# Optimization experiments

Hardware: AMD Instinct MI355X
Metric: run time of the kernel (lower is better)

The kernel has to match this reference:

```python
import jax, jax.numpy as jnp
import numpy as np

ALPHA = 0.2    # LeakyReLU negative slope (init arg alpha)
HEADS = 8
EPS = 1e-5     # LayerNorm eps


def setup_inputs() -> dict:
    key = jax.random.key(0)
    ks = jax.random.split(key, 16)
    B, S, D = 4, 1024, 256
    dh = D // HEADS  # 32
    x = jax.random.normal(ks[0], (B, S, D), jnp.float32)
    adj = (jax.random.uniform(ks[1], (B, S, S)) < 0.05).astype(jnp.float32)
    adj = jnp.maximum(adj, jnp.eye(S, dtype=jnp.float32)[None])

    def w(k, shape, fan):
        return jax.random.normal(k, shape, jnp.float32) * (fan ** -0.5)

    # GAT layer 0: in->hidden (concat heads)
    W0 = w(ks[2], (D, D), D); a_src0 = w(ks[3], (HEADS, dh), dh); a_dst0 = w(ks[4], (HEADS, dh), dh)
    # GAT layer 1: hidden->hidden (concat heads)
    W1 = w(ks[5], (D, D), D); a_src1 = w(ks[6], (HEADS, dh), dh); a_dst1 = w(ks[7], (HEADS, dh), dh)
    # GAT layer 2: hidden->out (mean over heads, head_dim = out_dim)
    W2 = w(ks[8], (D, HEADS * D), D); a_src2 = w(ks[9], (HEADS, D), D); a_dst2 = w(ks[10], (HEADS, D), D)
    # LayerNorm
    ln_g = jnp.ones((D,), jnp.float32); ln_b = jnp.zeros((D,), jnp.float32)
    # FFN: D -> 2D -> D
    ff_w1 = w(ks[11], (D, 2 * D), D); ff_b1 = jnp.zeros((2 * D,), jnp.float32)
    ff_w2 = w(ks[12], (2 * D, D), 2 * D); ff_b2 = jnp.zeros((D,), jnp.float32)
    return dict(adj=adj, x=x, W0=W0, a_src0=a_src0, a_dst0=a_dst0,
                W1=W1, a_src1=a_src1, a_dst1=a_dst1,
                W2=W2, a_src2=a_src2, a_dst2=a_dst2,
                ln_g=ln_g, ln_b=ln_b,
                ff_w1=ff_w1, ff_b1=ff_b1, ff_w2=ff_w2, ff_b2=ff_b2)


def _gat_layer(h, adj, W, a_src, a_dst, concat):
    B, S, _ = h.shape
    hp = jnp.einsum('bsi,io->bso', h, W).reshape(B, S, HEADS, -1)  # [B,S,H,dh]
    src = jnp.einsum('bshd,hd->bsh', hp, a_src)  # per-node source score
    dst = jnp.einsum('bshd,hd->bsh', hp, a_dst)  # per-node dest score
    # e[b,i,j,h] = LeakyReLU(src_i + dst_j), masked by adjacency
    e = jax.nn.leaky_relu(src[:, :, None, :] + dst[:, None, :, :], ALPHA)
    e = jnp.where(adj[..., None] > 0, e, jnp.float32(-1e9))
    attn = jax.nn.softmax(e, axis=2)  # softmax over neighbors j
    out = jnp.einsum('bijh,bjhd->bihd', attn, hp)
    return out.reshape(B, S, -1) if concat else out.mean(axis=2)


def reference(adj, x, W0, a_src0, a_dst0, W1, a_src1, a_dst1, W2, a_src2, a_dst2,
              ln_g, ln_b, ff_w1, ff_b1, ff_w2, ff_b2):
    # MultiAttentionGAT: 3 layers with residuals, ELU between layers
    h = jax.nn.elu(_gat_layer(x, adj, W0, a_src0, a_dst0, True) + x)
    h = jax.nn.elu(_gat_layer(h, adj, W1, a_src1, a_dst1, True) + h)
    h = _gat_layer(h, adj, W2, a_src2, a_dst2, False) + h
    # LayerNorm
    mu = h.mean(-1, keepdims=True)
    var = h.var(-1, keepdims=True)
    h = (h - mu) * jax.lax.rsqrt(var + EPS) * ln_g + ln_b
    # GELU FFN + residual
    ff = jnp.dot(jax.nn.gelu(jnp.dot(h, ff_w1) + ff_b1), ff_w2) + ff_b2
    return h + ff
```

## Files before the change

### kernel.cpp

```cpp
#include <hip/hip_runtime.h>
#include <hip/hip_bf16.h>

#define B_ 4
#define S_ 1024
#define D_ 256
#define H_ 8
#define LRELU_ALPHA 0.2f
#define MAXDEG 128

typedef __attribute__((ext_vector_type(8))) short short8;
typedef __attribute__((ext_vector_type(4))) float floatx4;

__device__ __forceinline__ float bf2f(unsigned short u) {
    union { unsigned int i; float f; } c; c.i = ((unsigned int)u) << 16; return c.f;
}
__device__ __forceinline__ unsigned short f2bf(float f) {
    union { float f; unsigned int u; } c; c.f = f;
    unsigned int r = (c.u + 0x7FFF + ((c.u >> 16) & 1)) >> 16;
    return (unsigned short)r;
}

__device__ void castT_body(const float* __restrict__ W, unsigned short* __restrict__ out,
                           int K, int N, int k0, int n0, float (*t)[33], int tid) {
    int tx = tid & 31, ty = tid >> 5;
#pragma unroll
    for (int i = 0; i < 4; ++i)
        t[ty + 8 * i][tx] = W[(size_t)(k0 + ty + 8 * i) * N + n0 + tx];
    __syncthreads();
#pragma unroll
    for (int i = 0; i < 4; ++i)
        out[(size_t)(n0 + ty + 8 * i) * K + k0 + tx] = f2bf(t[tx][ty + 8 * i]);
}

__global__ __launch_bounds__(256) void k_prep(
        const float* __restrict__ x, unsigned short* __restrict__ xb,
        const float* __restrict__ W0, unsigned short* __restrict__ W0t,
        const float* __restrict__ W1, unsigned short* __restrict__ W1t,
        const float* __restrict__ W2, unsigned short* __restrict__ W2t,
        const float* __restrict__ F1, unsigned short* __restrict__ F1t,
        const float* __restrict__ F2, unsigned short* __restrict__ F2t,
        const float* __restrict__ as2, const float* __restrict__ ad2,
        float* __restrict__ WS2, float* __restrict__ WD2,
        const float* __restrict__ adj, int* __restrict__ nbr, int* __restrict__ cnt) {
    __shared__ float t[32][33];
    __shared__ int c;
    int b = blockIdx.x, tid = threadIdx.x;
    if (b < 1024) {
        int i = b * 256 + tid;
        float4 v = ((const float4*)x)[i];
        ushort4 u; u.x = f2bf(v.x); u.y = f2bf(v.y); u.z = f2bf(v.z); u.w = f2bf(v.w);
        ((ushort4*)xb)[i] = u;
    } else if (b < 1088) {
        int i = b - 1024; castT_body(W0, W0t, 256, 256, (i & 7) * 32, (i >> 3) * 32, t, tid);
    } else if (b < 1152) {
        int i = b - 1088; castT_body(W1, W1t, 256, 256, (i & 7) * 32, (i >> 3) * 32, t, tid);
    } else if (b < 1664) {
        int i = b - 1152;
        int k0 = (i & 7) * 32, d0 = ((i >> 3) & 7) * 32, h = i >> 6;
        int tx = tid & 31, ty = tid >> 5;
#pragma unroll
        for (int q = 0; q < 4; ++q)
            t[ty + 8 * q][tx] = W2[(size_t)(k0 + ty + 8 * q) * 2048 + h * 256 + d0 + tx];
        __syncthreads();
#pragma unroll
        for (int q = 0; q < 4; ++q)
            W2t[(size_t)(d0 + ty + 8 * q) * 2048 + h * 256 + k0 + tx] = f2bf(t[tx][ty + 8 * q]);
    } else if (b < 1792) {
        int i = b - 1664; castT_body(F1, F1t, 256, 512, (i & 7) * 32, (i >> 3) * 32, t, tid);
    } else if (b < 1920) {
        int i = b - 1792; castT_body(F2, F2t, 512, 256, (i & 15) * 32, (i >> 4) * 32, t, tid);
    } else if (b < 2432) {
        int id = (b - 1920) * 4 + (tid >> 6);
        int h = id >> 8, k = id & 255;
        int lane = tid & 63;
        float4 w4 = *(const float4*)(W2 + (size_t)k * 2048 + h * 256 + lane * 4);
        float4 a4 = *(const float4*)(as2 + h * 256 + lane * 4);
        float4 d4 = *(const float4*)(ad2 + h * 256 + lane * 4);
        float s = w4.x * a4.x + w4.y * a4.y + w4.z * a4.z + w4.w * a4.w;
        float d = w4.x * d4.x + w4.y * d4.y + w4.z * d4.z + w4.w * d4.w;
#pragma unroll
        for (int o = 32; o; o >>= 1) { s += __shfl_xor(s, o); d += __shfl_xor(d, o); }
        if (lane == 0) { WS2[h * 256 + k] = s; WD2[h * 256 + k] = d; }
    } else {
        int row = b - 2432;
        if (tid == 0) c = 0;
        __syncthreads();
        float4 a4 = ((const float4*)(adj + (size_t)row * S_))[tid];
#pragma unroll
        for (int q = 0; q < 4; ++q) {
            float a = q == 0 ? a4.x : q == 1 ? a4.y : q == 2 ? a4.z : a4.w;
            if (a > 0.f) {
                int s = atomicAdd(&c, 1);
                if (s < MAXDEG) nbr[row * MAXDEG + s] = tid * 4 + q;
            }
        }
        __syncthreads();
        if (tid == 0) cnt[row] = c < MAXDEG ? c : MAXDEG;
    }
}

__global__ __launch_bounds__(256) void k_gemm_wide(const unsigned short* __restrict__ A,
        const unsigned short* __restrict__ Bt, float* __restrict__ P,
        int M, int N, int K, int Kc) {
    __shared__ unsigned short As[64][40];
    __shared__ unsigned short Bs[256][40];
    int tid = threadIdx.x;
    int bm = blockIdx.y * 64, bn = blockIdx.x * 256;
    int kbeg = blockIdx.z * Kc, kend = kbeg + Kc;
    int lane = tid & 63, wv = tid >> 6;
    int lrow = lane & 15, lq = lane >> 4;
    floatx4 acc[4][4] = {};
    int sm = tid >> 2, skq = (tid & 3) * 8;
    const unsigned short* Ap = A + (size_t)(bm + sm) * K + skq;
    const unsigned short* Bp0 = Bt + (size_t)(bn + sm) * K + skq;
    const unsigned short* Bp1 = Bp0 + (size_t)64 * K;
    const unsigned short* Bp2 = Bp0 + (size_t)128 * K;
    const unsigned short* Bp3 = Bp0 + (size_t)192 * K;
    short8 av  = *(const short8*)(Ap + kbeg);
    short8 bv0 = *(const short8*)(Bp0 + kbeg);
    short8 bv1 = *(const short8*)(Bp1 + kbeg);
    short8 bv2 = *(const short8*)(Bp2 + kbeg);
    short8 bv3 = *(const short8*)(Bp3 + kbeg);
    for (int k0 = kbeg; k0 < kend; k0 += 32) {
        *(short8*)&As[sm][skq]        = av;
        *(short8*)&Bs[sm][skq]        = bv0;
        *(short8*)&Bs[sm + 64][skq]   = bv1;
        *(short8*)&Bs[sm + 128][skq]  = bv2;
        *(short8*)&Bs[sm + 192][skq]  = bv3;
        __syncthreads();
        if (k0 + 32 < kend) {
            av  = *(const short8*)(Ap + k0 + 32);
            bv0 = *(const short8*)(Bp0 + k0 + 32);
            bv1 = *(const short8*)(Bp1 + k0 + 32);
            bv2 = *(const short8*)(Bp2 + k0 + 32);
            bv3 = *(const short8*)(Bp3 + k0 + 32);
        }
        short8 aF[4], bF[4];
#pragma unroll
        for (int mi = 0; mi < 4; ++mi)
            aF[mi] = *(const short8*)&As[mi * 16 + lrow][lq * 8];
#pragma unroll
        for (int ni = 0; ni < 4; ++ni)
            bF[ni] = *(const short8*)&Bs[wv * 64 + ni * 16 + lrow][lq * 8];
#pragma unroll
        for (int mi = 0; mi < 4; ++mi)
#pragma unroll
            for (int ni = 0; ni < 4; ++ni)
                acc[mi][ni] = __builtin_amdgcn_mfma_f32_16x16x32_bf16(aF[mi], bF[ni], acc[mi][ni], 0, 0, 0);
        __syncthreads();
    }
    float* out = P + (size_t)blockIdx.z * M * N;
#pragma unroll
    for (int mi = 0; mi < 4; ++mi)
#pragma unroll
        for (int ni = 0; ni < 4; ++ni)
#pragma unroll
            for (int r = 0; r < 4; ++r) {
                int grow = bm + mi * 16 + lq * 4 + r;
                int gcol = bn + wv * 64 + ni * 16 + lrow;
                out[(size_t)grow * N + gcol] = acc[mi][ni][r];
            }
}

template<int EPI>
__global__ __launch_bounds__(256) void k_gemm64(
        const unsigned short* __restrict__ A, const unsigned short* __restrict__ Bt,
        int N, int K,
        float* __restrict__ Pout, unsigned short* __restrict__ Ob,
        const float* __restrict__ p1, const float* __restrict__ p2,
        float* __restrict__ SRC, float* __restrict__ DST) {
    __shared__ unsigned short As[2][64][40];
    __shared__ unsigned short Bs[2][64][40];
    int tid = threadIdx.x;
    int bm = blockIdx.y * 64, bn = blockIdx.x * 64;
    int lane = tid & 63, wv = tid >> 6;
    int lrow = lane & 15, lq = lane >> 4;
    floatx4 acc[4] = {};
    int sm = tid >> 2, skq = (tid & 3) * 8;
    const unsigned short* Ap = A + (size_t)(bm + sm) * K + skq;
    const unsigned short* Bp = Bt + (size_t)(bn + sm) * K + skq;
    short8 av = *(const short8*)Ap;
    short8 bv = *(const short8*)Bp;
    *(short8*)&As[0][sm][skq] = av;
    *(short8*)&Bs[0][sm][skq] = bv;
    __syncthreads();
    int cur = 0;
    for (int k0 = 0; k0 < K; k0 += 32) {
        bool more = k0 + 32 < K;
        if (more) {
            av = *(const short8*)(Ap + k0 + 32);
            bv = *(const short8*)(Bp + k0 + 32);
        }
        short8 aF = *(const short8*)&As[cur][wv * 16 + lrow][lq * 8];
        short8 bF[4];
#pragma unroll
        for (int ni = 0; ni < 4; ++ni)
            bF[ni] = *(const short8*)&Bs[cur][ni * 16 + lrow][lq * 8];
#pragma unroll
        for (int ni = 0; ni < 4; ++ni)
            acc[ni] = __builtin_amdgcn_mfma_f32_16x16x32_bf16(aF, bF[ni], acc[ni], 0, 0, 0);
        if (more) {
            *(short8*)&As[cur ^ 1][sm][skq] = av;
            *(short8*)&Bs[cur ^ 1][sm][skq] = bv;
            __syncthreads();
            cur ^= 1;
        }
    }
    int row0 = bm + wv * 16 + lq * 4;
    if (EPI == 0) {
#pragma unroll
        for (int ni = 0; ni < 4; ++ni)
#pragma unroll
            for (int r = 0; r < 4; ++r)
                Ob[(size_t)(row0 + r) * N + bn + ni * 16 + lrow] = f2bf(acc[ni][r]);
        float asv[4], adv[4];
#pragma unroll
        for (int ni = 0; ni < 4; ++ni) {
            asv[ni] = p1[bn + ni * 16 + lrow];
            adv[ni] = p2[bn + ni * 16 + lrow];
        }
#pragma unroll
        for (int r = 0; r < 4; ++r) {
            float sA = acc[0][r] * asv[0] + acc[1][r] * asv[1];
            float sB = acc[2][r] * asv[2] + acc[3][r] * asv[3];
            float dA = acc[0][r] * adv[0] + acc[1][r] * adv[1];
            float dB = acc[2][r] * adv[2] + acc[3][r] * adv[3];
#pragma unroll
            for (int o = 8; o; o >>= 1) {
                sA += __shfl_xor(sA, o); sB += __shfl_xor(sB, o);
                dA += __shfl_xor(dA, o); dB += __shfl_xor(dB, o);
            }
            if (lrow == 0) {
                int h0 = bn >> 5;
                SRC[(row0 + r) * 8 + h0]     = sA;
                SRC[(row0 + r) * 8 + h0 + 1] = sB;
                DST[(row0 + r) * 8 + h0]     = dA;
                DST[(row0 + r) * 8 + h0 + 1] = dB;
            }
        }
    } else if (EPI == 2) {
#pragma unroll
        for (int ni = 0; ni < 4; ++ni) {
            int gcol = bn + ni * 16 + lrow;
            float bb = p1[gcol];
#pragma unroll
            for (int r = 0; r < 4; ++r) {
                float xx = acc[ni][r] + bb;
                float tt = tanhf(0.7978845608028654f * (xx + 0.044715f * xx * xx * xx));
                Ob[(size_t)(row0 + r) * N + gcol] = f2bf(0.5f * xx * (1.f + tt));
            }
        }
    } else if (EPI == 3) {
#pragma unroll
        for (int ni = 0; ni < 4; ++ni) {
            int gcol = bn + ni * 16 + lrow;
            float bb = p1[gcol];
#pragma unroll
            for (int r = 0; r < 4; ++r) {
                float res = p2[(size_t)(row0 + r) * 256 + gcol];
                Pout[(size_t)(row0 + r) * 256 + gcol] = acc[ni][r] + bb + res;
            }
        }
    }
}

__global__ __launch_bounds__(256) void k_attn4(const unsigned short* __restrict__ hp,
        const float* __restrict__ src, const float* __restrict__ dst,
        const int* __restrict__ nbr, const int* __restrict__ cnts,
        const float* __restrict__ X, float* __restrict__ Hout,
        unsigned short* __restrict__ Hb,
        const float* __restrict__ WS2, const float* __restrict__ WD2,
        float* __restrict__ SRC2, float* __restrict__ DST2) {
    int tid = threadIdx.x;
    int rq = tid >> 6;
    int lane = tid & 63;
    int row = blockIdx.x * 4 + rq;
    int rb = row & ~(S_ - 1);
    __shared__ int nb[4][MAXDEG];
    __shared__ float ss[4][8];
    __shared__ float ew[4][MAXDEG * 9];
    int cnt = cnts[row];
    for (int t = lane; t < cnt; t += 64) nb[rq][t] = nbr[row * MAXDEG + t];
    if (lane < 8) ss[rq][lane] = src[row * H_ + lane];
    for (int idx = lane; idx < cnt * 8; idx += 64) {
        int n = idx >> 3, h = idx & 7;
        int j = nb[rq][n];
        float e = ss[rq][h] + dst[(rb + j) * H_ + h];
        ew[rq][n * 9 + h] = e > 0.f ? e : LRELU_ALPHA * e;
    }
    {
        int h = lane >> 3, s8 = lane & 7;
        float m = -1e30f;
        for (int n = s8; n < cnt; n += 8) m = fmaxf(m, ew[rq][n * 9 + h]);
#pragma unroll
        for (int o = 4; o; o >>= 1) m = fmaxf(m, __shfl_xor(m, o));
        float s = 0.f;
        for (int n = s8; n < cnt; n += 8) {
            float v = __expf(ew[rq][n * 9 + h] - m); ew[rq][n * 9 + h] = v; s += v;
        }
#pragma unroll
        for (int o = 4; o; o >>= 1) s += __shfl_xor(s, o);
        float inv = s > 0.f ? 1.f / s : 0.f;
        for (int n = s8; n < cnt; n += 8) ew[rq][n * 9 + h] *= inv;
    }
    int d0 = lane * 4;
    int h = lane >> 3;
    const unsigned short* hpb = hp + (size_t)rb * 256 + d0;
    const float* ewr = ew[rq];
    float A0 = 0.f, A1 = 0.f, A2 = 0.f, A3 = 0.f;
    float B0 = 0.f, B1 = 0.f, B2 = 0.f, B3 = 0.f;
    int n = 0;
    for (; n + 3 < cnt; n += 4) {
        int j0 = nb[rq][n], j1 = nb[rq][n + 1];
        int j2 = nb[rq][n + 2], j3 = nb[rq][n + 3];
        uint2 p0 = *(const uint2*)(hpb + (size_t)j0 * 256);
        uint2 p1 = *(const uint2*)(hpb + (size_t)j1 * 256);
        uint2 p2 = *(const uint2*)(hpb + (size_t)j2 * 256);
        uint2 p3 = *(const uint2*)(hpb + (size_t)j3 * 256);
        float w0 = ewr[n * 9 + h], w1 = ewr[(n + 1) * 9 + h];
        float w2 = ewr[(n + 2) * 9 + h], w3 = ewr[(n + 3) * 9 + h];
        A0 += w0 * bf2f((unsigned short)p0.x); A1 += w0 * bf2f((unsigned short)(p0.x >> 16));
        A2 += w0 * bf2f((unsigned short)p0.y); A3 += w0 * bf2f((unsigned short)(p0.y >> 16));
        B0 += w1 * bf2f((unsigned short)p1.x); B1 += w1 * bf2f((unsigned short)(p1.x >> 16));
        B2 += w1 * bf2f((unsigned short)p1.y); B3 += w1 * bf2f((unsigned short)(p1.y >> 16));
        A0 += w2 * bf2f((unsigned short)p2.x); A1 += w2 * bf2f((unsigned short)(p2.x >> 16));
        A2 += w2 * bf2f((unsigned short)p2.y); A3 += w2 * bf2f((unsigned short)(p2.y >> 16));
        B0 += w3 * bf2f((unsigned short)p3.x); B1 += w3 * bf2f((unsigned short)(p3.x >> 16));
        B2 += w3 * bf2f((unsigned short)p3.y); B3 += w3 * bf2f((unsigned short)(p3.y >> 16));
    }
    for (; n < cnt; ++n) {
        int j = nb[rq][n];
        uint2 p = *(const uint2*)(hpb + (size_t)j * 256);
        float w = ewr[n * 9 + h];
        A0 += w * bf2f((unsigned short)p.x); A1 += w * bf2f((unsigned short)(p.x >> 16));
        A2 += w * bf2f((unsigned short)p.y); A3 += w * bf2f((unsigned short)(p.y >> 16));
    }
    float4 xv = *(const float4*)(X + (size_t)row * 256 + d0);
    float ov0 = A0 + B0 + xv.x;
    float ov1 = A1 + B1 + xv.y;
    float ov2 = A2 + B2 + xv.z;
    float ov3 = A3 + B3 + xv.w;
    ov0 = ov0 > 0.f ? ov0 : (__expf(ov0) - 1.f);
    ov1 = ov1 > 0.f ? ov1 : (__expf(ov1) - 1.f);
    ov2 = ov2 > 0.f ? ov2 : (__expf(ov2) - 1.f);
    ov3 = ov3 > 0.f ? ov3 : (__expf(ov3) - 1.f);
    *(float4*)(Hout + (size_t)row * 256 + d0) = make_float4(ov0, ov1, ov2, ov3);
    ushort4 ub; ub.x = f2bf(ov0); ub.y = f2bf(ov1); ub.z = f2bf(ov2); ub.w = f2bf(ov3);
    *(ushort4*)(Hb + (size_t)row * 256 + d0) = ub;
    if (WS2 != nullptr) {
#pragma unroll
        for (int hh = 0; hh < 8; ++hh) {
            float4 wsv = *(const float4*)(WS2 + hh * 256 + d0);
            float4 wdv = *(const float4*)(WD2 + hh * 256 + d0);
            float sP = ov0 * wsv.x + ov1 * wsv.y + ov2 * wsv.z + ov3 * wsv.w;
            float dP = ov0 * wdv.x + ov1 * wdv.y + ov2 * wdv.z + ov3 * wdv.w;
#pragma unroll
            for (int o = 32; o; o >>= 1) { sP += __shfl_xor(sP, o); dP += __shfl_xor(dP, o); }
            if (lane == 0) { SRC2[row * 8 + hh] = sP; DST2[row * 8 + hh] = dP; }
        }
    }
}

__global__ __launch_bounds__(256) void k_attn_Y(const unsigned short* __restrict__ Hb,
        const float* __restrict__ src2, const float* __restrict__ dst2,
        const int* __restrict__ nbr, const int* __restrict__ cnts,
        unsigned short* __restrict__ Ycat) {
    int tid = threadIdx.x;
    int half = tid >> 7, sub = tid & 127;
    int row = blockIdx.x * 2 + half;
    int rb = row & ~(S_ - 1);
    __shared__ int nb[2][MAXDEG];
    __shared__ float ss[2][8];
    __shared__ float ew[2][MAXDEG * 8];
    int cnt = cnts[row];
    for (int t = sub; t < cnt; t += 128) nb[half][t] = nbr[row * MAXDEG + t];
    if (sub < 8) ss[half][sub] = src2[row * H_ + sub];
    __syncthreads();
    for (int idx = sub; idx < cnt * 8; idx += 128) {
        int n = idx >> 3, h = idx & 7;
        int j = nb[half][n];
        float e = ss[half][h] + dst2[(rb + j) * H_ + h];
        ew[half][n * 8 + h] = e > 0.f ? e : LRELU_ALPHA * e;
    }
    __syncthreads();
    {
        int h = sub >> 4, s16 = sub & 15;
        float m = -1e30f;
        for (int n = s16; n < cnt; n += 16) m = fmaxf(m, ew[half][n * 8 + h]);
#pragma unroll
        for (int o = 8; o; o >>= 1) m = fmaxf(m, __shfl_xor(m, o));
        float s = 0.f;
        for (int n = s16; n < cnt; n += 16) {
            float v = __expf(ew[half][n * 8 + h] - m); ew[half][n * 8 + h] = v; s += v;
        }
#pragma unroll
        for (int o = 8; o; o >>= 1) s += __shfl_xor(s, o);
        float inv = s > 0.f ? 0.125f / s : 0.f;
        for (int n = s16; n < cnt; n += 16) ew[half][n * 8 + h] *= inv;
    }
    __syncthreads();
    const unsigned short* hbase = Hb + (size_t)rb * 256 + 2 * sub;
    const float* ewh = ew[half];
    float aA[8] = {}, aB[8] = {};
    int n = 0;
    for (; n + 1 < cnt; n += 2) {
        int j0 = nb[half][n], j1 = nb[half][n + 1];
        unsigned int p0 = *(const unsigned int*)(hbase + (size_t)j0 * 256);
        unsigned int p1 = *(const unsigned int*)(hbase + (size_t)j1 * 256);
        float4 w0a = *(const float4*)(ewh + n * 8);
        float4 w0b = *(const float4*)(ewh + n * 8 + 4);
        float4 w1a = *(const float4*)(ewh + (n + 1) * 8);
        float4 w1b = *(const float4*)(ewh + (n + 1) * 8 + 4);
        float v0a = bf2f((unsigned short)p0), v0b = bf2f((unsigned short)(p0 >> 16));
        float v1a = bf2f((unsigned short)p1), v1b = bf2f((unsigned short)(p1 >> 16));
        aA[0] += w0a.x * v0a + w1a.x * v1a;  aB[0] += w0a.x * v0b + w1a.x * v1b;
        aA[1] += w0a.y * v0a + w1a.y * v1a;  aB[1] += w0a.y * v0b + w1a.y * v1b;
        aA[2] += w0a.z * v0a + w1a.z * v1a;  aB[2] += w0a.z * v0b + w1a.z * v1b;
        aA[3] += w0a.w * v0a + w1a.w * v1a;  aB[3] += w0a.w * v0b + w1a.w * v1b;
        aA[4] += w0b.x * v0a + w1b.x * v1a;  aB[4] += w0b.x * v0b + w1b.x * v1b;
        aA[5] += w0b.y * v0a + w1b.y * v1a;  aB[5] += w0b.y * v0b + w1b.y * v1b;
        aA[6] += w0b.z * v0a + w1b.z * v1a;  aB[6] += w0b.z * v0b + w1b.z * v1b;
        aA[7] += w0b.w * v0a + w1b.w * v1a;  aB[7] += w0b.w * v0b + w1b.w * v1b;
    }
    for (; n < cnt; ++n) {
        int j = nb[half][n];
        unsigned int p = *(const unsigned int*)(hbase + (size_t)j * 256);
        float4 wa = *(const float4*)(ewh + n * 8);
        float4 wb = *(const float4*)(ewh + n * 8 + 4);
        float va = bf2f((unsigned short)p), vb = bf2f((unsigned short)(p >> 16));
        aA[0] += wa.x * va; aB[0] += wa.x * vb;
        aA[1] += wa.y * va; aB[1] += wa.y * vb;
        aA[2] += wa.z * va; aB[2] += wa.z * vb;
        aA[3] += wa.w * va; aB[3] += wa.w * vb;
        aA[4] += wb.x * va; aB[4] += wb.x * vb;
        aA[5] += wb.y * va; aB[5] += wb.y * vb;
        aA[6] += wb.z * va; aB[6] += wb.z * vb;
        aA[7] += wb.w * va; aB[7] += wb.w * vb;
    }
    unsigned short* yb = Ycat + (size_t)row * 2048 + 2 * sub;
#pragma unroll
    for (int hh = 0; hh < 8; ++hh) {
        ushort2 u; u.x = f2bf(aA[hh]); u.y = f2bf(aB[hh]);
        *(ushort2*)(yb + hh * 256) = u;
    }
}

__global__ __launch_bounds__(256) void k_ln_red(const float* __restrict__ P, int nsplit,
        const float* __restrict__ Hres, const float* __restrict__ g,
        const float* __restrict__ bta, float* __restrict__ HLN,
        unsigned short* __restrict__ HLNb) {
    int row = blockIdx.x * 4 + (threadIdx.x >> 6);
    int lane = threadIdx.x & 63;
    float4 v = ((const float4*)(Hres + (size_t)row * 256))[lane];
    for (int sp = 0; sp < nsplit; ++sp) {
        float4 p = ((const float4*)(P + (size_t)sp * 1048576 + (size_t)row * 256))[lane];
        v.x += p.x; v.y += p.y; v.z += p.z; v.w += p.w;
    }
    float s = v.x + v.y + v.z + v.w;
    float q = v.x * v.x + v.y * v.y + v.z * v.z + v.w * v.w;
    for (int o = 32; o; o >>= 1) { s += __shfl_xor(s, o); q += __shfl_xor(q, o); }
    float mu = s * (1.f / 256.f);
    float var = q * (1.f / 256.f) - mu * mu;
    if (var < 0.f) var = 0.f;
    float rs = rsqrtf(var + 1e-5f);
    float4 gg = ((const float4*)g)[lane];
    float4 bb = ((const float4*)bta)[lane];
    float4 o;
    o.x = (v.x - mu) * rs * gg.x + bb.x;
    o.y = (v.y - mu) * rs * gg.y + bb.y;
    o.z = (v.z - mu) * rs * gg.z + bb.z;
    o.w = (v.w - mu) * rs * gg.w + bb.w;
    ((float4*)(HLN + (size_t)row * 256))[lane] = o;
    ushort4 ob; ob.x = f2bf(o.x); ob.y = f2bf(o.y); ob.z = f2bf(o.z); ob.w = f2bf(o.w);
    ((ushort4*)(HLNb + (size_t)row * 256))[lane] = ob;
}

extern "C" void kernel_launch(void* const* d_in, const int* in_sizes, int n_in,
                              void* d_out, int out_size, void* d_ws, size_t ws_size,
                              hipStream_t stream) {
    const float* adj   = (const float*)d_in[0];
    const float* x     = (const float*)d_in[1];
    const float* W0    = (const float*)d_in[2];
    const float* as0   = (const float*)d_in[3];
    const float* ad0   = (const float*)d_in[4];
    const float* W1    = (const float*)d_in[5];
    const float* as1   = (const float*)d_in[6];
    const float* ad1   = (const float*)d_in[7];
    const float* W2    = (const float*)d_in[8];
    const float* as2   = (const float*)d_in[9];
    const float* ad2   = (const float*)d_in[10];
    const float* ln_g  = (const float*)d_in[11];
    const float* ln_b  = (const float*)d_in[12];
    const float* ff_w1 = (const float*)d_in[13];
    const float* ff_b1 = (const float*)d_in[14];
    const float* ff_w2 = (const float*)d_in[15];
    const float* ff_b2 = (const float*)d_in[16];

    float* ws = (float*)d_ws;
    float* H    = ws;
    float* HLN  = ws + 1048576;
    unsigned short* Ycat = (unsigned short*)(ws + 2097152);
    unsigned short* HPb  = (unsigned short*)(ws + 6291456);
    unsigned short* xb   = (unsigned short*)(ws + 6815744);
    unsigned short* Hb   = (unsigned short*)(ws + 7340032);
    unsigned short* HLNb = (unsigned short*)(ws + 7864320);
    unsigned short* MIDb = (unsigned short*)(ws + 8388608);
    unsigned short* W0t  = (unsigned short*)(ws + 9437184);
    unsigned short* W1t  = (unsigned short*)(ws + 9469952);
    unsigned short* W2t  = (unsigned short*)(ws + 9502720);
    unsigned short* F1t  = (unsigned short*)(ws + 9764864);
    unsigned short* F2t  = (unsigned short*)(ws + 9830400);
    float* WS2  = ws + 9895936;
    float* WD2  = ws + 9897984;
    float* SRC  = ws + 9900032;
    float* DST  = ws + 9932800;
    float* SRC2 = ws + 9965568;
    float* DST2 = ws + 9998336;
    int*   NBR  = (int*)(ws + 10031104);
    int*   CNT  = (int*)(ws + 10555392);
    float* PP   = ws + 12582912;

    k_prep<<<6528, 256, 0, stream>>>(x, xb, W0, W0t, W1, W1t, W2, W2t,
                                     ff_w1, F1t, ff_w2, F2t, as2, ad2, WS2, WD2,
                                     adj, NBR, CNT);

    k_gemm64<0><<<dim3(4, 64), 256, 0, stream>>>(xb, W0t, 256, 256,
                                                 nullptr, HPb, as0, ad0, SRC, DST);
    k_attn4<<<1024, 256, 0, stream>>>(HPb, SRC, DST, NBR, CNT, x, H, Hb,
                                      nullptr, nullptr, nullptr, nullptr);

    k_gemm64<0><<<dim3(4, 64), 256, 0, stream>>>(Hb, W1t, 256, 256,
                                                 nullptr, HPb, as1, ad1, SRC, DST);
    k_attn4<<<1024, 256, 0, stream>>>(HPb, SRC, DST, NBR, CNT, H, H, Hb,
                                      WS2, WD2, SRC2, DST2);

    k_attn_Y<<<2048, 256, 0, stream>>>(Hb, SRC2, DST2, NBR, CNT, Ycat);
    k_gemm_wide<<<dim3(1, 64, 8), 256, 0, stream>>>(Ycat, W2t, PP, 4096, 256, 2048, 256);
    k_ln_red<<<1024, 256, 0, stream>>>(PP, 8, H, ln_g, ln_b, HLN, HLNb);

    k_gemm64<2><<<dim3(8, 64), 256, 0, stream>>>(HLNb, F1t, 512, 256,
                                                 nullptr, MIDb, ff_b1, nullptr, nullptr, nullptr);
    k_gemm64<3><<<dim3(4, 64), 256, 0, stream>>>(MIDb, F2t, 256, 512,
                                                 (float*)d_out, nullptr, ff_b2, HLN, nullptr, nullptr);
}
```

Measured before the change: 214.3 us.

## Fuse W2 GEMM, LayerNorm and FFN into one per-row-block tail kernel

Replaces the split-K wide GEMM, the partial-sum reduce plus LayerNorm kernel, and both FFN GEMMs with a single kernel that owns 16 rows and keeps LN outputs and the GELU intermediate in LDS. This removes the split-K partial-sum traffic, the HLN/MID round-trips through global memory and three launches. The cost is that only 256 blocks of 512 threads run, each doing a long K=2048 loop with little per-block reuse and restreaming every weight matrix from L2 per block, which may lower parallelism and MFMA utilisation.

```diff
diff --git a/kernel.cpp b/kernel.cpp
--- a/kernel.cpp
+++ b/kernel.cpp
@@ -99,74 +99,10 @@
     }
 }
 
-__global__ __launch_bounds__(256) void k_gemm_wide(const unsigned short* __restrict__ A,
-        const unsigned short* __restrict__ Bt, float* __restrict__ P,
-        int M, int N, int K, int Kc) {
-    __shared__ unsigned short As[64][40];
-    __shared__ unsigned short Bs[256][40];
-    int tid = threadIdx.x;
-    int bm = blockIdx.y * 64, bn = blockIdx.x * 256;
-    int kbeg = blockIdx.z * Kc, kend = kbeg + Kc;
-    int lane = tid & 63, wv = tid >> 6;
-    int lrow = lane & 15, lq = lane >> 4;
-    floatx4 acc[4][4] = {};
-    int sm = tid >> 2, skq = (tid & 3) * 8;
-    const unsigned short* Ap = A + (size_t)(bm + sm) * K + skq;
-    const unsigned short* Bp0 = Bt + (size_t)(bn + sm) * K + skq;
-    const unsigned short* Bp1 = Bp0 + (size_t)64 * K;
-    const unsigned short* Bp2 = Bp0 + (size_t)128 * K;
-    const unsigned short* Bp3 = Bp0 + (size_t)192 * K;
-    short8 av  = *(const short8*)(Ap + kbeg);
-    short8 bv0 = *(const short8*)(Bp0 + kbeg);
-    short8 bv1 = *(const short8*)(Bp1 + kbeg);
-    short8 bv2 = *(const short8*)(Bp2 + kbeg);
-    short8 bv3 = *(const short8*)(Bp3 + kbeg);
-    for (int k0 = kbeg; k0 < kend; k0 += 32) {
-        *(short8*)&As[sm][skq]        = av;
-        *(short8*)&Bs[sm][skq]        = bv0;
-        *(short8*)&Bs[sm + 64][skq]   = bv1;
-        *(short8*)&Bs[sm + 128][skq]  = bv2;
-        *(short8*)&Bs[sm + 192][skq]  = bv3;
-        __syncthreads();
-        if (k0 + 32 < kend) {
-            av  = *(const short8*)(Ap + k0 + 32);
-            bv0 = *(const short8*)(Bp0 + k0 + 32);
-            bv1 = *(const short8*)(Bp1 + k0 + 32);
-            bv2 = *(const short8*)(Bp2 + k0 + 32);
-            bv3 = *(const short8*)(Bp3 + k0 + 32);
-        }
-        short8 aF[4], bF[4];
-#pragma unroll
-        for (int mi = 0; mi < 4; ++mi)
-            aF[mi] = *(const short8*)&As[mi * 16 + lrow][lq * 8];
-#pragma unroll
-        for (int ni = 0; ni < 4; ++ni)
-            bF[ni] = *(const short8*)&Bs[wv * 64 + ni * 16 + lrow][lq * 8];
-#pragma unroll
-        for (int mi = 0; mi < 4; ++mi)
-#pragma unroll
-            for (int ni = 0; ni < 4; ++ni)
-                acc[mi][ni] = __builtin_amdgcn_mfma_f32_16x16x32_bf16(aF[mi], bF[ni], acc[mi][ni], 0, 0, 0);
-        __syncthreads();
-    }
-    float* out = P + (size_t)blockIdx.z * M * N;
-#pragma unroll
-    for (int mi = 0; mi < 4; ++mi)
-#pragma unroll
-        for (int ni = 0; ni < 4; ++ni)
-#pragma unroll
-            for (int r = 0; r < 4; ++r) {
-                int grow = bm + mi * 16 + lq * 4 + r;
-                int gcol = bn + wv * 64 + ni * 16 + lrow;
-                out[(size_t)grow * N + gcol] = acc[mi][ni][r];
-            }
-}
-
-template<int EPI>
-__global__ __launch_bounds__(256) void k_gemm64(
+__global__ __launch_bounds__(256) void k_gemm64s(
         const unsigned short* __restrict__ A, const unsigned short* __restrict__ Bt,
         int N, int K,
-        float* __restrict__ Pout, unsigned short* __restrict__ Ob,
+        unsigned short* __restrict__ Ob,
         const float* __restrict__ p1, const float* __restrict__ p2,
         float* __restrict__ SRC, float* __restrict__ DST) {
     __shared__ unsigned short As[2][64][40];
@@ -207,59 +143,34 @@
         }
     }
     int row0 = bm + wv * 16 + lq * 4;
-    if (EPI == 0) {
-#pragma unroll
-        for (int ni = 0; ni < 4; ++ni)
-#pragma unroll
-            for (int r = 0; r < 4; ++r)
-                Ob[(size_t)(row0 + r) * N + bn + ni * 16 + lrow] = f2bf(acc[ni][r]);
-        float asv[4], adv[4];
-#pragma unroll
-        for (int ni = 0; ni < 4; ++ni) {
-            asv[ni] = p1[bn + ni * 16 + lrow];
-            adv[ni] = p2[bn + ni * 16 + lrow];
-        }
-#pragma unroll
-        for (int r = 0; r < 4; ++r) {
-            float sA = acc[0][r] * asv[0] + acc[1][r] * asv[1];
-            float sB = acc[2][r] * asv[2] + acc[3][r] * asv[3];
-            float dA = acc[0][r] * adv[0] + acc[1][r] * adv[1];
-            float dB = acc[2][r] * adv[2] + acc[3][r] * adv[3];
-#pragma unroll
-            for (int o = 8; o; o >>= 1) {
-                sA += __shfl_xor(sA, o); sB += __shfl_xor(sB, o);
-                dA += __shfl_xor(dA, o); dB += __shfl_xor(dB, o);
-            }
-            if (lrow == 0) {
-                int h0 = bn >> 5;
-                SRC[(row0 + r) * 8 + h0]     = sA;
-                SRC[(row0 + r) * 8 + h0 + 1] = sB;
-                DST[(row0 + r) * 8 + h0]     = dA;
-                DST[(row0 + r) * 8 + h0 + 1] = dB;
-            }
-        }
-    } else if (EPI == 2) {
-#pragma unroll
-        for (int ni = 0; ni < 4; ++ni) {
-            int gcol = bn + ni * 16 + lrow;
-            float bb = p1[gcol];
-#pragma unroll
-            for (int r = 0; r < 4; ++r) {
-                float xx = acc[ni][r] + bb;
-                float tt = tanhf(0.7978845608028654f * (xx + 0.044715f * xx * xx * xx));
-                Ob[(size_t)(row0 + r) * N + gcol] = f2bf(0.5f * xx * (1.f + tt));
-            }
-        }
-    } else if (EPI == 3) {
-#pragma unroll
-        for (int ni = 0; ni < 4; ++ni) {
-            int gcol = bn + ni * 16 + lrow;
-            float bb = p1[gcol];
-#pragma unroll
-            for (int r = 0; r < 4; ++r) {
-                float res = p2[(size_t)(row0 + r) * 256 + gcol];
-                Pout[(size_t)(row0 + r) * 256 + gcol] = acc[ni][r] + bb + res;
-            }
+#pragma unroll
+    for (int ni = 0; ni < 4; ++ni)
+#pragma unroll
+        for (int r = 0; r < 4; ++r)
+            Ob[(size_t)(row0 + r) * N + bn + ni * 16 + lrow] = f2bf(acc[ni][r]);
+    float asv[4], adv[4];
+#pragma unroll
+    for (int ni = 0; ni < 4; ++ni) {
+        asv[ni] = p1[bn + ni * 16 + lrow];
+        adv[ni] = p2[bn + ni * 16 + lrow];
+    }
+#pragma unroll
+    for (int r = 0; r < 4; ++r) {
+        float sA = acc[0][r] * asv[0] + acc[1][r] * asv[1];
+        float sB = acc[2][r] * asv[2] + acc[3][r] * asv[3];
+        float dA = acc[0][r] * adv[0] + acc[1][r] * adv[1];
+        float dB = acc[2][r] * adv[2] + acc[3][r] * adv[3];
+#pragma unroll
+        for (int o = 8; o; o >>= 1) {
+            sA += __shfl_xor(sA, o); sB += __shfl_xor(sB, o);
+            dA += __shfl_xor(dA, o); dB += __shfl_xor(dB, o);
+        }
+        if (lrow == 0) {
+            int h0 = bn >> 5;
+            SRC[(row0 + r) * 8 + h0]     = sA;
+            SRC[(row0 + r) * 8 + h0 + 1] = sB;
+            DST[(row0 + r) * 8 + h0]     = dA;
+            DST[(row0 + r) * 8 + h0 + 1] = dB;
         }
     }
 }
@@ -445,34 +356,179 @@
     }
 }
 
-__global__ __launch_bounds__(256) void k_ln_red(const float* __restrict__ P, int nsplit,
+union TailLDS {
+    struct { unsigned short As[2][16][40]; unsigned short Bs[2][256][40]; } p0;
+    struct { unsigned short alnb[16][264]; float hln[16][256];
+             unsigned short mid[16][520]; unsigned short Bs[256][40]; } p1;
+};
+
+__global__ __launch_bounds__(512) void k_tail(
+        const unsigned short* __restrict__ Ycat, const unsigned short* __restrict__ W2t,
         const float* __restrict__ Hres, const float* __restrict__ g,
-        const float* __restrict__ bta, float* __restrict__ HLN,
-        unsigned short* __restrict__ HLNb) {
-    int row = blockIdx.x * 4 + (threadIdx.x >> 6);
-    int lane = threadIdx.x & 63;
-    float4 v = ((const float4*)(Hres + (size_t)row * 256))[lane];
-    for (int sp = 0; sp < nsplit; ++sp) {
-        float4 p = ((const float4*)(P + (size_t)sp * 1048576 + (size_t)row * 256))[lane];
-        v.x += p.x; v.y += p.y; v.z += p.z; v.w += p.w;
-    }
-    float s = v.x + v.y + v.z + v.w;
-    float q = v.x * v.x + v.y * v.y + v.z * v.z + v.w * v.w;
-    for (int o = 32; o; o >>= 1) { s += __shfl_xor(s, o); q += __shfl_xor(q, o); }
-    float mu = s * (1.f / 256.f);
-    float var = q * (1.f / 256.f) - mu * mu;
-    if (var < 0.f) var = 0.f;
-    float rs = rsqrtf(var + 1e-5f);
-    float4 gg = ((const float4*)g)[lane];
-    float4 bb = ((const float4*)bta)[lane];
-    float4 o;
-    o.x = (v.x - mu) * rs * gg.x + bb.x;
-    o.y = (v.y - mu) * rs * gg.y + bb.y;
-    o.z = (v.z - mu) * rs * gg.z + bb.z;
-    o.w = (v.w - mu) * rs * gg.w + bb.w;
-    ((float4*)(HLN + (size_t)row * 256))[lane] = o;
-    ushort4 ob; ob.x = f2bf(o.x); ob.y = f2bf(o.y); ob.z = f2bf(o.z); ob.w = f2bf(o.w);
-    ((ushort4*)(HLNb + (size_t)row * 256))[lane] = ob;
+        const float* __restrict__ bta,
+        const unsigned short* __restrict__ F1t, const float* __restrict__ b1,
+        const unsigned short* __restrict__ F2t, const float* __restrict__ b2,
+        float* __restrict__ out) {
+    __shared__ TailLDS u;
+    __shared__ float red[8][16][2];
+    __shared__ float mv[16][2];
+    int tid = threadIdx.x;
+    int lane = tid & 63, wv = tid >> 6;
+    int lrow = lane & 15, lq = lane >> 4;
+    int r0 = blockIdx.x * 16;
+    int sm = tid >> 1, skq = (tid & 1) * 16;
+    int colb = wv * 32 + lrow;
+
+    const unsigned short* Bp = W2t + (size_t)sm * 2048 + skq;
+    const unsigned short* Ayp = Ycat + (size_t)(r0 + sm) * 2048 + skq;
+    floatx4 acc0[2] = {};
+    short8 bva = *(const short8*)Bp;
+    short8 bvb = *(const short8*)(Bp + 8);
+    short8 ava, avb;
+    if (tid < 32) { ava = *(const short8*)Ayp; avb = *(const short8*)(Ayp + 8); }
+    *(short8*)&u.p0.Bs[0][sm][skq]     = bva;
+    *(short8*)&u.p0.Bs[0][sm][skq + 8] = bvb;
+    if (tid < 32) {
+        *(short8*)&u.p0.As[0][sm][skq]     = ava;
+        *(short8*)&u.p0.As[0][sm][skq + 8] = avb;
+    }
+    __syncthreads();
+    int cur = 0;
+    for (int s = 0; s < 64; ++s) {
+        int k0 = s * 32;
+        bool more = s < 63;
+        if (more) {
+            bva = *(const short8*)(Bp + k0 + 32);
+            bvb = *(const short8*)(Bp + k0 + 40);
+            if (tid < 32) {
+                ava = *(const short8*)(Ayp + k0 + 32);
+                avb = *(const short8*)(Ayp + k0 + 40);
+            }
+        }
+        short8 aF  = *(const short8*)&u.p0.As[cur][lrow][lq * 8];
+        short8 bF0 = *(const short8*)&u.p0.Bs[cur][wv * 32 + lrow][lq * 8];
+        short8 bF1 = *(const short8*)&u.p0.Bs[cur][wv * 32 + 16 + lrow][lq * 8];
+        acc0[0] = __builtin_amdgcn_mfma_f32_16x16x32_bf16(aF, bF0, acc0[0], 0, 0, 0);
+        acc0[1] = __builtin_amdgcn_mfma_f32_16x16x32_bf16(aF, bF1, acc0[1], 0, 0, 0);
+        if (more) {
+            *(short8*)&u.p0.Bs[cur ^ 1][sm][skq]     = bva;
+            *(short8*)&u.p0.Bs[cur ^ 1][sm][skq + 8] = bvb;
+            if (tid < 32) {
+                *(short8*)&u.p0.As[cur ^ 1][sm][skq]     = ava;
+                *(short8*)&u.p0.As[cur ^ 1][sm][skq + 8] = avb;
+            }
+            __syncthreads();
+            cur ^= 1;
+        }
+    }
+    float v0[4], v1[4];
+#pragma unroll
+    for (int r = 0; r < 4; ++r) {
+        int row = lq * 4 + r;
+        v0[r] = acc0[0][r] + Hres[(size_t)(r0 + row) * 256 + colb];
+        v1[r] = acc0[1][r] + Hres[(size_t)(r0 + row) * 256 + colb + 16];
+    }
+    float ps[4], pq[4];
+#pragma unroll
+    for (int r = 0; r < 4; ++r) {
+        ps[r] = v0[r] + v1[r];
+        pq[r] = v0[r] * v0[r] + v1[r] * v1[r];
+    }
+#pragma unroll
+    for (int o = 1; o < 16; o <<= 1)
+#pragma unroll
+        for (int r = 0; r < 4; ++r) {
+            ps[r] += __shfl_xor(ps[r], o);
+            pq[r] += __shfl_xor(pq[r], o);
+        }
+    if (lrow == 0)
+#pragma unroll
+        for (int r = 0; r < 4; ++r) {
+            red[wv][lq * 4 + r][0] = ps[r];
+            red[wv][lq * 4 + r][1] = pq[r];
+        }
+    __syncthreads();
+    if (tid < 16) {
+        float s = 0.f, q = 0.f;
+#pragma unroll
+        for (int w = 0; w < 8; ++w) { s += red[w][tid][0]; q += red[w][tid][1]; }
+        float mu = s * (1.f / 256.f);
+        float var = q * (1.f / 256.f) - mu * mu;
+        if (var < 0.f) var = 0.f;
+        mv[tid][0] = mu;
+        mv[tid][1] = rsqrtf(var + 1e-5f);
+    }
+    __syncthreads();
+    {
+        float gv0 = g[colb], gv1 = g[colb + 16];
+        float bv0f = bta[colb], bv1f = bta[colb + 16];
+#pragma unroll
+        for (int r = 0; r < 4; ++r) {
+            int row = lq * 4 + r;
+            float mu = mv[row][0], rs = mv[row][1];
+            float h0 = (v0[r] - mu) * rs * gv0 + bv0f;
+            float h1 = (v1[r] - mu) * rs * gv1 + bv1f;
+            u.p1.hln[row][colb]       = h0;
+            u.p1.hln[row][colb + 16]  = h1;
+            u.p1.alnb[row][colb]      = f2bf(h0);
+            u.p1.alnb[row][colb + 16] = f2bf(h1);
+        }
+    }
+    __syncthreads();
+
+#pragma unroll 1
+    for (int hf = 0; hf < 2; ++hf) {
+        floatx4 acc1[2] = {};
+        const unsigned short* Fp = F1t + (size_t)(hf * 256 + sm) * 256 + skq;
+        for (int s = 0; s < 8; ++s) {
+            int k0 = s * 32;
+            *(short8*)&u.p1.Bs[sm][skq]     = *(const short8*)(Fp + k0);
+            *(short8*)&u.p1.Bs[sm][skq + 8] = *(const short8*)(Fp + k0 + 8);
+            __syncthreads();
+            short8 aF  = *(const short8*)&u.p1.alnb[lrow][k0 + lq * 8];
+            short8 bF0 = *(const short8*)&u.p1.Bs[wv * 32 + lrow][lq * 8];
+            short8 bF1 = *(const short8*)&u.p1.Bs[wv * 32 + 16 + lrow][lq * 8];
+            acc1[0] = __builtin_amdgcn_mfma_f32_16x16x32_bf16(aF, bF0, acc1[0], 0, 0, 0);
+            acc1[1] = __builtin_amdgcn_mfma_f32_16x16x32_bf16(aF, bF1, acc1[1], 0, 0, 0);
+            __syncthreads();
+        }
+#pragma unroll
+        for (int ni = 0; ni < 2; ++ni) {
+            int gcol = hf * 256 + colb + ni * 16;
+            float bb = b1[gcol];
+#pragma unroll
+            for (int r = 0; r < 4; ++r) {
+                float xx = acc1[ni][r] + bb;
+                float tt = tanhf(0.7978845608028654f * (xx + 0.044715f * xx * xx * xx));
+                u.p1.mid[lq * 4 + r][gcol] = f2bf(0.5f * xx * (1.f + tt));
+            }
+        }
+    }
+
+    floatx4 acc2[2] = {};
+    const unsigned short* F2p = F2t + (size_t)sm * 512 + skq;
+    for (int s = 0; s < 16; ++s) {
+        int k0 = s * 32;
+        *(short8*)&u.p1.Bs[sm][skq]     = *(const short8*)(F2p + k0);
+        *(short8*)&u.p1.Bs[sm][skq + 8] = *(const short8*)(F2p + k0 + 8);
+        __syncthreads();
+        short8 aF  = *(const short8*)&u.p1.mid[lrow][k0 + lq * 8];
+        short8 bF0 = *(const short8*)&u.p1.Bs[wv * 32 + lrow][lq * 8];
+        short8 bF1 = *(const short8*)&u.p1.Bs[wv * 32 + 16 + lrow][lq * 8];
+        acc2[0] = __builtin_amdgcn_mfma_f32_16x16x32_bf16(aF, bF0, acc2[0], 0, 0, 0);
+        acc2[1] = __builtin_amdgcn_mfma_f32_16x16x32_bf16(aF, bF1, acc2[1], 0, 0, 0);
+        __syncthreads();
+    }
+#pragma unroll
+    for (int ni = 0; ni < 2; ++ni) {
+        int col = colb + ni * 16;
+        float bb = b2[col];
+#pragma unroll
+        for (int r = 0; r < 4; ++r) {
+            int row = lq * 4 + r;
+            out[(size_t)(r0 + row) * 256 + col] = acc2[ni][r] + bb + u.p1.hln[row][col];
+        }
+    }
 }
 
 extern "C" void kernel_launch(void* const* d_in, const int* in_sizes, int n_in,
@@ -498,13 +554,10 @@
 
     float* ws = (float*)d_ws;
     float* H    = ws;
-    float* HLN  = ws + 1048576;
     unsigned short* Ycat = (unsigned short*)(ws + 2097152);
     unsigned short* HPb  = (unsigned short*)(ws + 6291456);
     unsigned short* xb   = (unsigned short*)(ws + 6815744);
     unsigned short* Hb   = (unsigned short*)(ws + 7340032);
-    unsigned short* HLNb = (unsigned short*)(ws + 7864320);
-    unsigned short* MIDb = (unsigned short*)(ws + 8388608);
     unsigned short* W0t  = (unsigned short*)(ws + 9437184);
     unsigned short* W1t  = (unsigned short*)(ws + 9469952);
     unsigned short* W2t  = (unsigned short*)(ws + 9502720);
@@ -518,28 +571,20 @@
     float* DST2 = ws + 9998336;
     int*   NBR  = (int*)(ws + 10031104);
     int*   CNT  = (int*)(ws + 10555392);
-    float* PP   = ws + 12582912;
 
     k_prep<<<6528, 256, 0, stream>>>(x, xb, W0, W0t, W1, W1t, W2, W2t,
                                      ff_w1, F1t, ff_w2, F2t, as2, ad2, WS2, WD2,
                                      adj, NBR, CNT);
 
-    k_gemm64<0><<<dim3(4, 64), 256, 0, stream>>>(xb, W0t, 256, 256,
-                                                 nullptr, HPb, as0, ad0, SRC, DST);
+    k_gemm64s<<<dim3(4, 64), 256, 0, stream>>>(xb, W0t, 256, 256, HPb, as0, ad0, SRC, DST);
     k_attn4<<<1024, 256, 0, stream>>>(HPb, SRC, DST, NBR, CNT, x, H, Hb,
                                       nullptr, nullptr, nullptr, nullptr);
 
-    k_gemm64<0><<<dim3(4, 64), 256, 0, stream>>>(Hb, W1t, 256, 256,
-                                                 nullptr, HPb, as1, ad1, SRC, DST);
+    k_gemm64s<<<dim3(4, 64), 256, 0, stream>>>(Hb, W1t, 256, 256, HPb, as1, ad1, SRC, DST);
     k_attn4<<<1024, 256, 0, stream>>>(HPb, SRC, DST, NBR, CNT, H, H, Hb,
                                       WS2, WD2, SRC2, DST2);
 
     k_attn_Y<<<2048, 256, 0, stream>>>(Hb, SRC2, DST2, NBR, CNT, Ycat);
-    k_gemm_wide<<<dim3(1, 64, 8), 256, 0, stream>>>(Ycat, W2t, PP, 4096, 256, 2048, 256);
-    k_ln_red<<<1024, 256, 0, stream>>>(PP, 8, H, ln_g, ln_b, HLN, HLNb);
-
-    k_gemm64<2><<<dim3(8, 64), 256, 0, stream>>>(HLNb, F1t, 512, 256,
-                                                 nullptr, MIDb, ff_b1, nullptr, nullptr, nullptr);
-    k_gemm64<3><<<dim3(4, 64), 256, 0, stream>>>(MIDb, F2t, 256, 512,
-                                                 (float*)d_out, nullptr, ff_b2, HLN, nullptr, nullptr);
-}
+    k_tail<<<256, 512, 0, stream>>>(Ycat, W2t, H, ln_g, ln_b,
+                                    F1t, ff_b1, F2t, ff_b2, (float*)d_out);
+}
```

Result: slower. 249.7 us (+16.5%).

## Replace split-K wide GEMM with full-K 64x64 GEMM fusing residual add

Applied to the files above, without the earlier changes.

The layer-2 projection GEMM (M=4096, N=256, K=2048) previously ran as an 8-way split-K wide-tile kernel writing eight partial fp32 outputs, which the LayerNorm kernel then summed together with the residual. It now uses the 64x64 tile GEMM over the full K with an epilogue that adds the residual, and LayerNorm reads a single combined buffer. This removes the partial-sum writes and reads (8 x 4 MB) but drops from 512 blocks to 256 blocks, each doing a long K loop, which lowers parallelism.

```diff
diff --git a/kernel.cpp b/kernel.cpp
--- a/kernel.cpp
+++ b/kernel.cpp
@@ -97,69 +97,6 @@
         __syncthreads();
         if (tid == 0) cnt[row] = c < MAXDEG ? c : MAXDEG;
     }
-}
-
-__global__ __launch_bounds__(256) void k_gemm_wide(const unsigned short* __restrict__ A,
-        const unsigned short* __restrict__ Bt, float* __restrict__ P,
-        int M, int N, int K, int Kc) {
-    __shared__ unsigned short As[64][40];
-    __shared__ unsigned short Bs[256][40];
-    int tid = threadIdx.x;
-    int bm = blockIdx.y * 64, bn = blockIdx.x * 256;
-    int kbeg = blockIdx.z * Kc, kend = kbeg + Kc;
-    int lane = tid & 63, wv = tid >> 6;
-    int lrow = lane & 15, lq = lane >> 4;
-    floatx4 acc[4][4] = {};
-    int sm = tid >> 2, skq = (tid & 3) * 8;
-    const unsigned short* Ap = A + (size_t)(bm + sm) * K + skq;
-    const unsigned short* Bp0 = Bt + (size_t)(bn + sm) * K + skq;
-    const unsigned short* Bp1 = Bp0 + (size_t)64 * K;
-    const unsigned short* Bp2 = Bp0 + (size_t)128 * K;
-    const unsigned short* Bp3 = Bp0 + (size_t)192 * K;
-    short8 av  = *(const short8*)(Ap + kbeg);
-    short8 bv0 = *(const short8*)(Bp0 + kbeg);
-    short8 bv1 = *(const short8*)(Bp1 + kbeg);
-    short8 bv2 = *(const short8*)(Bp2 + kbeg);
-    short8 bv3 = *(const short8*)(Bp3 + kbeg);
-    for (int k0 = kbeg; k0 < kend; k0 += 32) {
-        *(short8*)&As[sm][skq]        = av;
-        *(short8*)&Bs[sm][skq]        = bv0;
-        *(short8*)&Bs[sm + 64][skq]   = bv1;
-        *(short8*)&Bs[sm + 128][skq]  = bv2;
-        *(short8*)&Bs[sm + 192][skq]  = bv3;
-        __syncthreads();
-        if (k0 + 32 < kend) {
-            av  = *(const short8*)(Ap + k0 + 32);
-            bv0 = *(const short8*)(Bp0 + k0 + 32);
-            bv1 = *(const short8*)(Bp1 + k0 + 32);
-            bv2 = *(const short8*)(Bp2 + k0 + 32);
-            bv3 = *(const short8*)(Bp3 + k0 + 32);
-        }
-        short8 aF[4], bF[4];
-#pragma unroll
-        for (int mi = 0; mi < 4; ++mi)
-            aF[mi] = *(const short8*)&As[mi * 16 + lrow][lq * 8];
-#pragma unroll
-        for (int ni = 0; ni < 4; ++ni)
-            bF[ni] = *(const short8*)&Bs[wv * 64 + ni * 16 + lrow][lq * 8];
-#pragma unroll
-        for (int mi = 0; mi < 4; ++mi)
-#pragma unroll
-            for (int ni = 0; ni < 4; ++ni)
-                acc[mi][ni] = __builtin_amdgcn_mfma_f32_16x16x32_bf16(aF[mi], bF[ni], acc[mi][ni], 0, 0, 0);
-        __syncthreads();
-    }
-    float* out = P + (size_t)blockIdx.z * M * N;
-#pragma unroll
-    for (int mi = 0; mi < 4; ++mi)
-#pragma unroll
-        for (int ni = 0; ni < 4; ++ni)
-#pragma unroll
-            for (int r = 0; r < 4; ++r) {
-                int grow = bm + mi * 16 + lq * 4 + r;
-                int gcol = bn + wv * 64 + ni * 16 + lrow;
-                out[(size_t)grow * N + gcol] = acc[mi][ni][r];
-            }
 }
 
 template<int EPI>
@@ -238,6 +175,16 @@
                 DST[(row0 + r) * 8 + h0 + 1] = dB;
             }
         }
+    } else if (EPI == 1) {
+#pragma unroll
+        for (int ni = 0; ni < 4; ++ni) {
+            int gcol = bn + ni * 16 + lrow;
+#pragma unroll
+            for (int r = 0; r < 4; ++r) {
+                float res = p2[(size_t)(row0 + r) * 256 + gcol];
+                Pout[(size_t)(row0 + r) * 256 + gcol] = acc[ni][r] + res;
+            }
+        }
     } else if (EPI == 2) {
 #pragma unroll
         for (int ni = 0; ni < 4; ++ni) {
@@ -445,17 +392,12 @@
     }
 }
 
-__global__ __launch_bounds__(256) void k_ln_red(const float* __restrict__ P, int nsplit,
-        const float* __restrict__ Hres, const float* __restrict__ g,
-        const float* __restrict__ bta, float* __restrict__ HLN,
-        unsigned short* __restrict__ HLNb) {
+__global__ __launch_bounds__(256) void k_ln2(const float* __restrict__ CH,
+        const float* __restrict__ g, const float* __restrict__ bta,
+        float* __restrict__ HLN, unsigned short* __restrict__ HLNb) {
     int row = blockIdx.x * 4 + (threadIdx.x >> 6);
     int lane = threadIdx.x & 63;
-    float4 v = ((const float4*)(Hres + (size_t)row * 256))[lane];
-    for (int sp = 0; sp < nsplit; ++sp) {
-        float4 p = ((const float4*)(P + (size_t)sp * 1048576 + (size_t)row * 256))[lane];
-        v.x += p.x; v.y += p.y; v.z += p.z; v.w += p.w;
-    }
+    float4 v = ((const float4*)(CH + (size_t)row * 256))[lane];
     float s = v.x + v.y + v.z + v.w;
     float q = v.x * v.x + v.y * v.y + v.z * v.z + v.w * v.w;
     for (int o = 32; o; o >>= 1) { s += __shfl_xor(s, o); q += __shfl_xor(q, o); }
@@ -518,7 +460,7 @@
     float* DST2 = ws + 9998336;
     int*   NBR  = (int*)(ws + 10031104);
     int*   CNT  = (int*)(ws + 10555392);
-    float* PP   = ws + 12582912;
+    float* CH   = ws + 12582912;
 
     k_prep<<<6528, 256, 0, stream>>>(x, xb, W0, W0t, W1, W1t, W2, W2t,
                                      ff_w1, F1t, ff_w2, F2t, as2, ad2, WS2, WD2,
@@ -535,8 +477,9 @@
                                       WS2, WD2, SRC2, DST2);
 
     k_attn_Y<<<2048, 256, 0, stream>>>(Hb, SRC2, DST2, NBR, CNT, Ycat);
-    k_gemm_wide<<<dim3(1, 64, 8), 256, 0, stream>>>(Ycat, W2t, PP, 4096, 256, 2048, 256);
-    k_ln_red<<<1024, 256, 0, stream>>>(PP, 8, H, ln_g, ln_b, HLN, HLNb);
+    k_gemm64<1><<<dim3(4, 64), 256, 0, stream>>>(Ycat, W2t, 256, 2048,
+                                                 CH, nullptr, nullptr, H, nullptr, nullptr);
+    k_ln2<<<1024, 256, 0, stream>>>(CH, ln_g, ln_b, HLN, HLNb);
 
     k_gemm64<2><<<dim3(8, 64), 256, 0, stream>>>(HLNb, F1t, 512, 256,
                                                  nullptr, MIDb, ff_b1, nullptr, nullptr, nullptr);
```

Result: slower. 222.7 us (+4.0%).
